# Kernel tuning notes

Measured on AMD Instinct MI355X. Metric: run time of the kernel, lower is better.

## Reference

```python
import jax, jax.numpy as jnp
import numpy as np

B, N, H = 32, 512, 128
LN_EPS = 1e-5

def _layernorm(x):
    # LayerNorm over last dim, no affine (elementwise_affine=False)
    mu = jnp.mean(x, axis=-1, keepdims=True)
    var = jnp.var(x, axis=-1, keepdims=True)
    return (x - mu) * jax.lax.rsqrt(var + LN_EPS)

def setup_inputs() -> dict:
    key = jax.random.key(0)
    k0, k1, k2, k3 = jax.random.split(key, 4)
    s = jax.random.normal(k0, (B, N, H), dtype=jnp.float32)
    ev = jax.random.normal(k1, (B, N, N, 3), dtype=jnp.float32)
    mask = (jax.random.uniform(k2, (B, N, N, 1)) > 0.5).astype(jnp.float32)
    W1 = jax.random.normal(k3, (H, H), dtype=jnp.float32) / np.sqrt(H)
    b1 = jnp.zeros((H,), dtype=jnp.float32)
    return {"s": s, "ev": ev, "mask": mask, "W1": W1, "b1": b1}

def reference(s, ev, mask, W1, b1):
    # lin1: Linear -> LayerNorm (no affine) -> SiLU
    h = jnp.einsum('bnh,kh->bnk', s, W1) + b1          # (B, N, H)
    h = jax.nn.silu(_layernorm(h))
    # Fused CFConv: v[b,i,c,d] = sum_j mask[b,i,j] * ev[b,i,j,c] * h[b,j,d]
    mev = ev * mask                                     # (B, N, N, 3)
    v = jnp.einsum('bijc,bjd->bicd', mev, h)            # (B, N, 3, H)
    return v
```

## Files before the change

kernel.cpp:

```cpp
#include <hip/hip_runtime.h>
#include <hip/hip_bf16.h>

#define B_ 32
#define N_ 512
#define H_ 128

typedef float f32x4 __attribute__((ext_vector_type(4)));
typedef short short8 __attribute__((ext_vector_type(8)));
typedef short short4v __attribute__((ext_vector_type(4)));

static __device__ __forceinline__ float bf2f(unsigned short u) {
  union { unsigned int ui; float f; } x;
  x.ui = ((unsigned int)u) << 16;
  return x.f;
}
static __device__ __forceinline__ unsigned short f2bf(float f) {
  __hip_bfloat16 h = __float2bfloat16(f);
  return *reinterpret_cast<unsigned short*>(&h);
}

__global__ __launch_bounds__(256) void lin_ln_silu_kernel(
    const float* __restrict__ s, const float* __restrict__ W1,
    const float* __restrict__ b1, unsigned short* __restrict__ h_t) {
  __shared__ float s_sh[32 * 132];
  __shared__ unsigned short w_sh[128 * 132];
  __shared__ unsigned short ht_sh[128 * 40];
  const int t = threadIdx.x;
  const int b = blockIdx.y;
  const int n0 = blockIdx.x * 32;

#pragma unroll
  for (int r = 0; r < 16; ++r) {
    int q = t + 256 * r;
    int d = q >> 5, part = q & 31;
    float4 v = *reinterpret_cast<const float4*>(W1 + d * H_ + part * 4);
    short4v w;
    w.x = (short)f2bf(v.x); w.y = (short)f2bf(v.y);
    w.z = (short)f2bf(v.z); w.w = (short)f2bf(v.w);
    *reinterpret_cast<short4v*>(&w_sh[d * 132 + part * 4]) = w;
  }
#pragma unroll
  for (int r = 0; r < 4; ++r) {
    int q = t + 256 * r;
    int n = q >> 5, part = q & 31;
    float4 v = *reinterpret_cast<const float4*>(
        s + ((size_t)b * N_ + n0 + n) * H_ + part * 4);
    *reinterpret_cast<float4*>(&s_sh[n * 132 + part * 4]) = v;
  }
  __syncthreads();

  const int a = t & 15;
  const int g = t >> 4;
  float acc[2][8];
#pragma unroll
  for (int nn = 0; nn < 2; ++nn)
#pragma unroll
    for (int dd = 0; dd < 8; ++dd) acc[nn][dd] = 0.f;

  float bias[8];
#pragma unroll
  for (int dd = 0; dd < 8; ++dd) bias[dd] = b1[dd * 16 + a];

  for (int k = 0; k < 128; k += 4) {
    float wf[8][4];
#pragma unroll
    for (int dd = 0; dd < 8; ++dd) {
      short4v wv =
          *reinterpret_cast<const short4v*>(&w_sh[(dd * 16 + a) * 132 + k]);
      wf[dd][0] = bf2f((unsigned short)wv.x);
      wf[dd][1] = bf2f((unsigned short)wv.y);
      wf[dd][2] = bf2f((unsigned short)wv.z);
      wf[dd][3] = bf2f((unsigned short)wv.w);
    }
#pragma unroll
    for (int nn = 0; nn < 2; ++nn) {
      float4 sv =
          *reinterpret_cast<const float4*>(&s_sh[(nn * 16 + g) * 132 + k]);
#pragma unroll
      for (int dd = 0; dd < 8; ++dd) {
        acc[nn][dd] += sv.x * wf[dd][0] + sv.y * wf[dd][1] +
                       sv.z * wf[dd][2] + sv.w * wf[dd][3];
      }
    }
  }

#pragma unroll
  for (int nn = 0; nn < 2; ++nn) {
    float s1 = 0.f, s2 = 0.f;
#pragma unroll
    for (int dd = 0; dd < 8; ++dd) {
      float x = acc[nn][dd] + bias[dd];
      acc[nn][dd] = x;
      s1 += x;
      s2 += x * x;
    }
#pragma unroll
    for (int off = 8; off >= 1; off >>= 1) {
      s1 += __shfl_xor(s1, off);
      s2 += __shfl_xor(s2, off);
    }
    float mean = s1 * (1.f / 128.f);
    float var = s2 * (1.f / 128.f) - mean * mean;
    float rs = rsqrtf(var + 1e-5f);
#pragma unroll
    for (int dd = 0; dd < 8; ++dd) {
      float x = (acc[nn][dd] - mean) * rs;
      float y = x / (1.f + __expf(-x));
      ht_sh[(dd * 16 + a) * 40 + nn * 16 + g] = f2bf(y);
    }
  }
  __syncthreads();

#pragma unroll
  for (int r = 0; r < 2; ++r) {
    int q = t + 256 * r;
    int d = q >> 2, part = q & 3;
    float4 v = *reinterpret_cast<const float4*>(&ht_sh[d * 40 + part * 8]);
    *reinterpret_cast<float4*>(
        h_t + ((size_t)b * 128 + d) * 512 + n0 + part * 8) = v;
  }
}

__global__ __launch_bounds__(256) void cfconv_mfma_kernel(
    const float* __restrict__ ev, const float* __restrict__ mask,
    const unsigned short* __restrict__ h_t, float* __restrict__ out) {
  __shared__ unsigned short ph[48 * 72];
  __shared__ unsigned short hh[128 * 72];
  const int t = threadIdx.x;
  const int b = blockIdx.y;
  const int i0 = blockIdx.x * 16;
  const int lane = t & 63;
  const int w = t >> 6;
  const int l15 = lane & 15;
  const int quad = lane >> 4;

  f32x4 acc[3][2];
#pragma unroll
  for (int mt = 0; mt < 3; ++mt)
#pragma unroll
    for (int nt = 0; nt < 2; ++nt)
#pragma unroll
      for (int e = 0; e < 4; ++e) acc[mt][nt][e] = 0.f;

  for (int j0 = 0; j0 < N_; j0 += 64) {
    __syncthreads();

#pragma unroll
    for (int r = 0; r < 4; ++r) {
      int q = t + 256 * r;
      int d = q >> 3, p8 = q & 7;
      float4 v = *reinterpret_cast<const float4*>(
          h_t + ((size_t)b * 128 + d) * 512 + j0 + p8 * 8);
      *reinterpret_cast<float4*>(&hh[d * 72 + p8 * 8]) = v;
    }

#pragma unroll
    for (int r = 0; r < 3; ++r) {
      int q = t + 256 * r;
      int i = q / 48, part = q % 48;
      int f0 = part * 4;
      const float* evbase =
          ev + ((size_t)((b * N_ + i0 + i)) * N_ + j0) * 3;
      float4 e4 = *reinterpret_cast<const float4*>(evbase + f0);
      const float* mrow = mask + (size_t)(b * N_ + i0 + i) * N_ + j0;
      int jlo = f0 / 3, jhi = (f0 + 3) / 3;
      float mlo = mrow[jlo], mhi = mrow[jhi];
      float evv[4] = {e4.x, e4.y, e4.z, e4.w};
#pragma unroll
      for (int e = 0; e < 4; ++e) {
        int f = f0 + e;
        int j = f / 3, c = f - 3 * j;
        float m = (j == jlo) ? mlo : mhi;
        ph[(c * 16 + i) * 72 + j] = f2bf(evv[e] * m);
      }
    }
    __syncthreads();

#pragma unroll
    for (int ks = 0; ks < 2; ++ks) {
      short8 av[3], bv[2];
#pragma unroll
      for (int mt = 0; mt < 3; ++mt)
        av[mt] = *reinterpret_cast<const short8*>(
            &ph[(mt * 16 + l15) * 72 + ks * 32 + quad * 8]);
#pragma unroll
      for (int nt = 0; nt < 2; ++nt) {
        int d = w * 32 + nt * 16 + l15;
        bv[nt] = *reinterpret_cast<const short8*>(
            &hh[d * 72 + ks * 32 + quad * 8]);
      }
#pragma unroll
      for (int mt = 0; mt < 3; ++mt)
#pragma unroll
        for (int nt = 0; nt < 2; ++nt)
          acc[mt][nt] = __builtin_amdgcn_mfma_f32_16x16x32_bf16(
              av[mt], bv[nt], acc[mt][nt], 0, 0, 0);
    }
  }

#pragma unroll
  for (int mt = 0; mt < 3; ++mt) {
#pragma unroll
    for (int nt = 0; nt < 2; ++nt) {
      int d = w * 32 + nt * 16 + l15;
#pragma unroll
      for (int r = 0; r < 4; ++r) {
        int i = i0 + quad * 4 + r;
        out[(((size_t)b * N_ + i) * 3 + mt) * H_ + d] = acc[mt][nt][r];
      }
    }
  }
}

extern "C" void kernel_launch(void* const* d_in, const int* in_sizes, int n_in,
                              void* d_out, int out_size, void* d_ws,
                              size_t ws_size, hipStream_t stream) {
  const float* s = (const float*)d_in[0];
  const float* ev = (const float*)d_in[1];
  const float* mask = (const float*)d_in[2];
  const float* W1 = (const float*)d_in[3];
  const float* b1 = (const float*)d_in[4];
  float* out = (float*)d_out;
  unsigned short* h_t = (unsigned short*)d_ws;

  lin_ln_silu_kernel<<<dim3(N_ / 32, B_), 256, 0, stream>>>(s, W1, b1, h_t);
  cfconv_mfma_kernel<<<dim3(N_ / 16, B_), 256, 0, stream>>>(ev, mask, h_t, out);
}
```

Measured before the change: 214.1 us.

## Split CFConv feature dim across blocks and vectorize ev/mask staging loads

The CFConv kernel now launches two 128-thread blocks per (batch, 16-row) tile, each covering half of the 128 feature columns, which doubles the grid and halves the shared h tile. The ev/mask staging is rewritten so each thread loads three float4 of ev and one float4 of mask for four j values, then writes packed short4 bf16 values per channel instead of scalar stores. The aim is more parallelism, wider global loads and fewer scattered LDS writes. In exchange, every ev/mask tile is now read and converted twice, once by each feature-half block, which adds HBM/L2 traffic on the dominant input.

```diff
diff --git a/kernel.cpp b/kernel.cpp
--- a/kernel.cpp
+++ b/kernel.cpp
@@ -121,14 +121,15 @@
   }
 }
 
-__global__ __launch_bounds__(256) void cfconv_mfma_kernel(
+__global__ __launch_bounds__(128) void cfconv_mfma_kernel(
     const float* __restrict__ ev, const float* __restrict__ mask,
     const unsigned short* __restrict__ h_t, float* __restrict__ out) {
   __shared__ unsigned short ph[48 * 72];
-  __shared__ unsigned short hh[128 * 72];
+  __shared__ unsigned short hh[64 * 72];
   const int t = threadIdx.x;
-  const int b = blockIdx.y;
-  const int i0 = blockIdx.x * 16;
+  const int dhalf = blockIdx.x * 64;
+  const int i0 = blockIdx.y * 16;
+  const int b = blockIdx.z;
   const int lane = t & 63;
   const int w = t >> 6;
   const int l15 = lane & 15;
@@ -147,31 +148,36 @@
 
 #pragma unroll
     for (int r = 0; r < 4; ++r) {
-      int q = t + 256 * r;
+      int q = t + 128 * r;
       int d = q >> 3, p8 = q & 7;
       float4 v = *reinterpret_cast<const float4*>(
-          h_t + ((size_t)b * 128 + d) * 512 + j0 + p8 * 8);
+          h_t + ((size_t)b * 128 + dhalf + d) * 512 + j0 + p8 * 8);
       *reinterpret_cast<float4*>(&hh[d * 72 + p8 * 8]) = v;
     }
 
 #pragma unroll
-    for (int r = 0; r < 3; ++r) {
-      int q = t + 256 * r;
-      int i = q / 48, part = q % 48;
-      int f0 = part * 4;
-      const float* evbase =
-          ev + ((size_t)((b * N_ + i0 + i)) * N_ + j0) * 3;
-      float4 e4 = *reinterpret_cast<const float4*>(evbase + f0);
-      const float* mrow = mask + (size_t)(b * N_ + i0 + i) * N_ + j0;
-      int jlo = f0 / 3, jhi = (f0 + 3) / 3;
-      float mlo = mrow[jlo], mhi = mrow[jhi];
-      float evv[4] = {e4.x, e4.y, e4.z, e4.w};
-#pragma unroll
-      for (int e = 0; e < 4; ++e) {
-        int f = f0 + e;
-        int j = f / 3, c = f - 3 * j;
-        float m = (j == jlo) ? mlo : mhi;
-        ph[(c * 16 + i) * 72 + j] = f2bf(evv[e] * m);
+    for (int r = 0; r < 2; ++r) {
+      int task = t + 128 * r;
+      int i = task >> 4, jq = task & 15;
+      int j = jq * 4;
+      const float* evb =
+          ev + ((size_t)(b * N_ + i0 + i) * N_ + j0 + j) * 3;
+      float4 e0 = *reinterpret_cast<const float4*>(evb);
+      float4 e1 = *reinterpret_cast<const float4*>(evb + 4);
+      float4 e2 = *reinterpret_cast<const float4*>(evb + 8);
+      float4 m4 = *reinterpret_cast<const float4*>(
+          mask + (size_t)(b * N_ + i0 + i) * N_ + j0 + j);
+      float f[12] = {e0.x, e0.y, e0.z, e0.w, e1.x, e1.y,
+                     e1.z, e1.w, e2.x, e2.y, e2.z, e2.w};
+      float mm[4] = {m4.x, m4.y, m4.z, m4.w};
+#pragma unroll
+      for (int c = 0; c < 3; ++c) {
+        short4v wv;
+        wv.x = (short)f2bf(f[0 * 3 + c] * mm[0]);
+        wv.y = (short)f2bf(f[1 * 3 + c] * mm[1]);
+        wv.z = (short)f2bf(f[2 * 3 + c] * mm[2]);
+        wv.w = (short)f2bf(f[3 * 3 + c] * mm[3]);
+        *reinterpret_cast<short4v*>(&ph[(c * 16 + i) * 72 + j]) = wv;
       }
     }
     __syncthreads();
@@ -202,7 +208,7 @@
   for (int mt = 0; mt < 3; ++mt) {
 #pragma unroll
     for (int nt = 0; nt < 2; ++nt) {
-      int d = w * 32 + nt * 16 + l15;
+      int d = dhalf + w * 32 + nt * 16 + l15;
 #pragma unroll
       for (int r = 0; r < 4; ++r) {
         int i = i0 + quad * 4 + r;
@@ -224,5 +230,6 @@
   unsigned short* h_t = (unsigned short*)d_ws;
 
   lin_ln_silu_kernel<<<dim3(N_ / 32, B_), 256, 0, stream>>>(s, W1, b1, h_t);
-  cfconv_mfma_kernel<<<dim3(N_ / 16, B_), 256, 0, stream>>>(ev, mask, h_t, out);
-}
+  cfconv_mfma_kernel<<<dim3(2, N_ / 16, B_), 128, 0, stream>>>(ev, mask, h_t,
+                                                               out);
+}
```

Result: no change. 214.9 us (+0.4%).

## Use MFMA for linear layer and store h in pre-swizzled MFMA fragment layout

Applied to the files above, without the earlier changes.

The first kernel now converts s and W1 to bf16 in MFMA fragment order and computes the linear layer with bf16 MFMA instead of scalar FMA. LayerNorm statistics are reduced across two waves through shared memory. h is written in a fragment-ready global layout, so the cfconv kernel loads B operands straight from global without staging them in LDS. The cfconv grid is split over d-halves with 128-thread blocks. The split means each block re-reads the ev/mask tile, doubling that traffic, and the s input is now rounded to bf16.

```diff
diff --git a/kernel.cpp b/kernel.cpp
--- a/kernel.cpp
+++ b/kernel.cpp
@@ -9,207 +9,215 @@
 typedef short short8 __attribute__((ext_vector_type(8)));
 typedef short short4v __attribute__((ext_vector_type(4)));
 
-static __device__ __forceinline__ float bf2f(unsigned short u) {
-  union { unsigned int ui; float f; } x;
-  x.ui = ((unsigned int)u) << 16;
-  return x.f;
-}
 static __device__ __forceinline__ unsigned short f2bf(float f) {
   __hip_bfloat16 h = __float2bfloat16(f);
   return *reinterpret_cast<unsigned short*>(&h);
 }
 
-__global__ __launch_bounds__(256) void lin_ln_silu_kernel(
+
+__global__ __launch_bounds__(256, 2) void lin_ln_silu_kernel(
     const float* __restrict__ s, const float* __restrict__ W1,
-    const float* __restrict__ b1, unsigned short* __restrict__ h_t) {
-  __shared__ float s_sh[32 * 132];
-  __shared__ unsigned short w_sh[128 * 132];
-  __shared__ unsigned short ht_sh[128 * 40];
+    const float* __restrict__ b1, unsigned short* __restrict__ hfrag) {
+  __shared__ unsigned short afr[2 * 4 * 512];
+  __shared__ unsigned short bfr[8 * 4 * 512];
+  __shared__ unsigned short trans[128 * 34];
+  __shared__ float lnb[2][32][2];
   const int t = threadIdx.x;
+  const int n0 = blockIdx.x * 32;
   const int b = blockIdx.y;
-  const int n0 = blockIdx.x * 32;
-
-#pragma unroll
-  for (int r = 0; r < 16; ++r) {
-    int q = t + 256 * r;
-    int d = q >> 5, part = q & 31;
-    float4 v = *reinterpret_cast<const float4*>(W1 + d * H_ + part * 4);
-    short4v w;
-    w.x = (short)f2bf(v.x); w.y = (short)f2bf(v.y);
-    w.z = (short)f2bf(v.z); w.w = (short)f2bf(v.w);
-    *reinterpret_cast<short4v*>(&w_sh[d * 132 + part * 4]) = w;
-  }
-#pragma unroll
-  for (int r = 0; r < 4; ++r) {
-    int q = t + 256 * r;
-    int n = q >> 5, part = q & 31;
-    float4 v = *reinterpret_cast<const float4*>(
-        s + ((size_t)b * N_ + n0 + n) * H_ + part * 4);
-    *reinterpret_cast<float4*>(&s_sh[n * 132 + part * 4]) = v;
-  }
-  __syncthreads();
-
-  const int a = t & 15;
-  const int g = t >> 4;
-  float acc[2][8];
-#pragma unroll
-  for (int nn = 0; nn < 2; ++nn)
-#pragma unroll
-    for (int dd = 0; dd < 8; ++dd) acc[nn][dd] = 0.f;
-
-  float bias[8];
-#pragma unroll
-  for (int dd = 0; dd < 8; ++dd) bias[dd] = b1[dd * 16 + a];
-
-  for (int k = 0; k < 128; k += 4) {
-    float wf[8][4];
-#pragma unroll
-    for (int dd = 0; dd < 8; ++dd) {
-      short4v wv =
-          *reinterpret_cast<const short4v*>(&w_sh[(dd * 16 + a) * 132 + k]);
-      wf[dd][0] = bf2f((unsigned short)wv.x);
-      wf[dd][1] = bf2f((unsigned short)wv.y);
-      wf[dd][2] = bf2f((unsigned short)wv.z);
-      wf[dd][3] = bf2f((unsigned short)wv.w);
-    }
-#pragma unroll
-    for (int nn = 0; nn < 2; ++nn) {
-      float4 sv =
-          *reinterpret_cast<const float4*>(&s_sh[(nn * 16 + g) * 132 + k]);
-#pragma unroll
-      for (int dd = 0; dd < 8; ++dd) {
-        acc[nn][dd] += sv.x * wf[dd][0] + sv.y * wf[dd][1] +
-                       sv.z * wf[dd][2] + sv.w * wf[dd][3];
-      }
-    }
-  }
-
-#pragma unroll
-  for (int nn = 0; nn < 2; ++nn) {
-    float s1 = 0.f, s2 = 0.f;
-#pragma unroll
-    for (int dd = 0; dd < 8; ++dd) {
-      float x = acc[nn][dd] + bias[dd];
-      acc[nn][dd] = x;
-      s1 += x;
-      s2 += x * x;
-    }
-#pragma unroll
-    for (int off = 8; off >= 1; off >>= 1) {
-      s1 += __shfl_xor(s1, off);
-      s2 += __shfl_xor(s2, off);
-    }
-    float mean = s1 * (1.f / 128.f);
-    float var = s2 * (1.f / 128.f) - mean * mean;
-    float rs = rsqrtf(var + 1e-5f);
-#pragma unroll
-    for (int dd = 0; dd < 8; ++dd) {
-      float x = (acc[nn][dd] - mean) * rs;
-      float y = x / (1.f + __expf(-x));
-      ht_sh[(dd * 16 + a) * 40 + nn * 16 + g] = f2bf(y);
-    }
-  }
-  __syncthreads();
-
-#pragma unroll
-  for (int r = 0; r < 2; ++r) {
-    int q = t + 256 * r;
-    int d = q >> 2, part = q & 3;
-    float4 v = *reinterpret_cast<const float4*>(&ht_sh[d * 40 + part * 8]);
-    *reinterpret_cast<float4*>(
-        h_t + ((size_t)b * 128 + d) * 512 + n0 + part * 8) = v;
-  }
-}
-
-__global__ __launch_bounds__(256) void cfconv_mfma_kernel(
-    const float* __restrict__ ev, const float* __restrict__ mask,
-    const unsigned short* __restrict__ h_t, float* __restrict__ out) {
-  __shared__ unsigned short ph[48 * 72];
-  __shared__ unsigned short hh[128 * 72];
-  const int t = threadIdx.x;
-  const int b = blockIdx.y;
-  const int i0 = blockIdx.x * 16;
   const int lane = t & 63;
   const int w = t >> 6;
   const int l15 = lane & 15;
   const int quad = lane >> 4;
 
+#pragma unroll
+  for (int rep = 0; rep < 4; ++rep) {
+    int q = t + 256 * rep;
+    int n = q >> 5, k = (q & 31) * 4;
+    float4 v = *reinterpret_cast<const float4*>(
+        s + ((size_t)(b * N_ + n0 + n)) * H_ + k);
+    short4v sv;
+    sv.x = (short)f2bf(v.x); sv.y = (short)f2bf(v.y);
+    sv.z = (short)f2bf(v.z); sv.w = (short)f2bf(v.w);
+    int mt = n >> 4, ks = k >> 5, qd = (k >> 3) & 3, e0 = k & 7;
+    *reinterpret_cast<short4v*>(
+        &afr[((mt * 4 + ks) * 64 + qd * 16 + (n & 15)) * 8 + e0]) = sv;
+  }
+#pragma unroll
+  for (int rep = 0; rep < 16; ++rep) {
+    int q = t + 256 * rep;
+    int d = q >> 5, k = (q & 31) * 4;
+    float4 v = *reinterpret_cast<const float4*>(W1 + (size_t)d * H_ + k);
+    short4v sv;
+    sv.x = (short)f2bf(v.x); sv.y = (short)f2bf(v.y);
+    sv.z = (short)f2bf(v.z); sv.w = (short)f2bf(v.w);
+    int nt = d >> 4, ks = k >> 5, qd = (k >> 3) & 3, e0 = k & 7;
+    *reinterpret_cast<short4v*>(
+        &bfr[((nt * 4 + ks) * 64 + qd * 16 + (d & 15)) * 8 + e0]) = sv;
+  }
+  __syncthreads();
+
+  const int mt = w >> 1, dhalf = w & 1;
+  f32x4 acc[4];
+#pragma unroll
+  for (int nt2 = 0; nt2 < 4; ++nt2)
+#pragma unroll
+    for (int e = 0; e < 4; ++e) acc[nt2][e] = 0.f;
+
+#pragma unroll
+  for (int ks = 0; ks < 4; ++ks) {
+    short8 av =
+        *reinterpret_cast<const short8*>(&afr[((mt * 4 + ks) * 64 + lane) * 8]);
+#pragma unroll
+    for (int nt2 = 0; nt2 < 4; ++nt2) {
+      short8 bv = *reinterpret_cast<const short8*>(
+          &bfr[(((dhalf * 4 + nt2) * 4 + ks) * 64 + lane) * 8]);
+      acc[nt2] =
+          __builtin_amdgcn_mfma_f32_16x16x32_bf16(av, bv, acc[nt2], 0, 0, 0);
+    }
+  }
+
+  float bb[4];
+#pragma unroll
+  for (int nt2 = 0; nt2 < 4; ++nt2)
+    bb[nt2] = b1[dhalf * 64 + nt2 * 16 + l15];
+
+#pragma unroll
+  for (int rr = 0; rr < 4; ++rr) {
+    float s1 = 0.f, s2 = 0.f;
+#pragma unroll
+    for (int nt2 = 0; nt2 < 4; ++nt2) {
+      float x = acc[nt2][rr] + bb[nt2];
+      acc[nt2][rr] = x;
+      s1 += x;
+      s2 += x * x;
+    }
+#pragma unroll
+    for (int off = 8; off >= 1; off >>= 1) {
+      s1 += __shfl_xor(s1, off);
+      s2 += __shfl_xor(s2, off);
+    }
+    int row = mt * 16 + quad * 4 + rr;
+    if (l15 == 0) {
+      lnb[dhalf][row][0] = s1;
+      lnb[dhalf][row][1] = s2;
+    }
+  }
+  __syncthreads();
+
+#pragma unroll
+  for (int rr = 0; rr < 4; ++rr) {
+    int row = mt * 16 + quad * 4 + rr;
+    float s1 = lnb[0][row][0] + lnb[1][row][0];
+    float s2 = lnb[0][row][1] + lnb[1][row][1];
+    float mean = s1 * (1.f / 128.f);
+    float var = s2 * (1.f / 128.f) - mean * mean;
+    float rs = rsqrtf(var + 1e-5f);
+#pragma unroll
+    for (int nt2 = 0; nt2 < 4; ++nt2) {
+      float x = (acc[nt2][rr] - mean) * rs;
+      float y = x / (1.f + __expf(-x));
+      trans[(dhalf * 64 + nt2 * 16 + l15) * 34 + row] = f2bf(y);
+    }
+  }
+  __syncthreads();
+
+#pragma unroll
+  for (int rep = 0; rep < 2; ++rep) {
+    int q = t + 256 * rep;
+    int d = q >> 2, k2 = q & 3;
+    short8 v = *reinterpret_cast<const short8*>(&trans[d * 34 + k2 * 8]);
+    int n = n0 + k2 * 8;
+    int KS = n >> 5, q16 = (n >> 3) & 3;
+    *reinterpret_cast<short8*>(
+        hfrag + (size_t)b * 65536 +
+        (size_t)(((d >> 4) * 16 + KS) * 64 + q16 * 16 + (d & 15)) * 8) = v;
+  }
+}
+
+__global__ __launch_bounds__(128, 5) void cfconv_mfma_kernel(
+    const float* __restrict__ ev, const float* __restrict__ mask,
+    const unsigned short* __restrict__ hfrag, float* __restrict__ out) {
+  __shared__ unsigned short ph[3 * 2 * 512];
+  const int t = threadIdx.x;
+  const int i0 = blockIdx.x * 16;
+  const int dh4 = blockIdx.y * 4;
+  const int b = blockIdx.z;
+  const int lane = t & 63;
+  const int w = t >> 6;
+  const int l15 = lane & 15;
+  const int quad = lane >> 4;
+
+  const float* evb = ev + (size_t)(b * N_ + i0) * N_ * 3;
+  const float* mb = mask + (size_t)(b * N_ + i0) * N_;
+  const unsigned short* hfb = hfrag + (size_t)b * 65536;
+
   f32x4 acc[3][2];
 #pragma unroll
-  for (int mt = 0; mt < 3; ++mt)
-#pragma unroll
-    for (int nt = 0; nt < 2; ++nt)
-#pragma unroll
-      for (int e = 0; e < 4; ++e) acc[mt][nt][e] = 0.f;
-
-  for (int j0 = 0; j0 < N_; j0 += 64) {
-    __syncthreads();
-
-#pragma unroll
-    for (int r = 0; r < 4; ++r) {
-      int q = t + 256 * r;
-      int d = q >> 3, p8 = q & 7;
-      float4 v = *reinterpret_cast<const float4*>(
-          h_t + ((size_t)b * 128 + d) * 512 + j0 + p8 * 8);
-      *reinterpret_cast<float4*>(&hh[d * 72 + p8 * 8]) = v;
-    }
-
-#pragma unroll
-    for (int r = 0; r < 3; ++r) {
-      int q = t + 256 * r;
-      int i = q / 48, part = q % 48;
-      int f0 = part * 4;
-      const float* evbase =
-          ev + ((size_t)((b * N_ + i0 + i)) * N_ + j0) * 3;
-      float4 e4 = *reinterpret_cast<const float4*>(evbase + f0);
-      const float* mrow = mask + (size_t)(b * N_ + i0 + i) * N_ + j0;
-      int jlo = f0 / 3, jhi = (f0 + 3) / 3;
-      float mlo = mrow[jlo], mhi = mrow[jhi];
-      float evv[4] = {e4.x, e4.y, e4.z, e4.w};
+  for (int c = 0; c < 3; ++c)
+#pragma unroll
+    for (int p = 0; p < 2; ++p)
+#pragma unroll
+      for (int e = 0; e < 4; ++e) acc[c][p][e] = 0.f;
+
+  for (int r = 0; r < 8; ++r) {
+    const int j0 = r * 64;
+    if (r) __syncthreads();
+
+#pragma unroll
+    for (int rep = 0; rep < 6; ++rep) {
+      int ch = t + 128 * rep;
+      int i = ch / 48;
+      int f0 = (ch % 48) * 4;
+      float4 e4 = *reinterpret_cast<const float4*>(
+          evb + ((size_t)i * N_ + j0) * 3 + f0);
+      int jl0 = f0 / 3;
+      float mlo = mb[(size_t)i * N_ + j0 + jl0];
+      float mhi = mb[(size_t)i * N_ + j0 + jl0 + 1];
+      float fe[4] = {e4.x, e4.y, e4.z, e4.w};
 #pragma unroll
       for (int e = 0; e < 4; ++e) {
         int f = f0 + e;
-        int j = f / 3, c = f - 3 * j;
-        float m = (j == jlo) ? mlo : mhi;
-        ph[(c * 16 + i) * 72 + j] = f2bf(evv[e] * m);
+        int j = f / 3;
+        int c = f - j * 3;
+        float m = (j == jl0) ? mlo : mhi;
+        ph[c * 1024 + (j >> 5) * 512 + ((j >> 3) & 3) * 128 + i * 8 +
+           (j & 7)] = f2bf(fe[e] * m);
       }
     }
     __syncthreads();
 
 #pragma unroll
     for (int ks = 0; ks < 2; ++ks) {
-      short8 av[3], bv[2];
-#pragma unroll
-      for (int mt = 0; mt < 3; ++mt)
-        av[mt] = *reinterpret_cast<const short8*>(
-            &ph[(mt * 16 + l15) * 72 + ks * 32 + quad * 8]);
-#pragma unroll
-      for (int nt = 0; nt < 2; ++nt) {
-        int d = w * 32 + nt * 16 + l15;
-        bv[nt] = *reinterpret_cast<const short8*>(
-            &hh[d * 72 + ks * 32 + quad * 8]);
+      short8 av[3];
+#pragma unroll
+      for (int c = 0; c < 3; ++c)
+        av[c] = *reinterpret_cast<const short8*>(
+            &ph[(c * 2 + ks) * 512 + lane * 8]);
+#pragma unroll
+      for (int p = 0; p < 2; ++p) {
+        const int NT = dh4 + w * 2 + p;
+        short8 bv = *reinterpret_cast<const short8*>(
+            hfb + (size_t)((NT * 16 + r * 2 + ks) * 64 + lane) * 8);
+#pragma unroll
+        for (int c = 0; c < 3; ++c)
+          acc[c][p] = __builtin_amdgcn_mfma_f32_16x16x32_bf16(av[c], bv,
+                                                              acc[c][p], 0, 0, 0);
       }
-#pragma unroll
-      for (int mt = 0; mt < 3; ++mt)
-#pragma unroll
-        for (int nt = 0; nt < 2; ++nt)
-          acc[mt][nt] = __builtin_amdgcn_mfma_f32_16x16x32_bf16(
-              av[mt], bv[nt], acc[mt][nt], 0, 0, 0);
-    }
-  }
-
-#pragma unroll
-  for (int mt = 0; mt < 3; ++mt) {
-#pragma unroll
-    for (int nt = 0; nt < 2; ++nt) {
-      int d = w * 32 + nt * 16 + l15;
-#pragma unroll
-      for (int r = 0; r < 4; ++r) {
-        int i = i0 + quad * 4 + r;
-        out[(((size_t)b * N_ + i) * 3 + mt) * H_ + d] = acc[mt][nt][r];
+    }
+  }
+
+#pragma unroll
+  for (int c = 0; c < 3; ++c)
+#pragma unroll
+    for (int p = 0; p < 2; ++p) {
+      const int d = (dh4 + w * 2 + p) * 16 + l15;
+#pragma unroll
+      for (int rr = 0; rr < 4; ++rr) {
+        const int i = i0 + quad * 4 + rr;
+        out[(((size_t)b * N_ + i) * 3 + c) * H_ + d] = acc[c][p][rr];
       }
     }
-  }
 }
 
 extern "C" void kernel_launch(void* const* d_in, const int* in_sizes, int n_in,
@@ -221,8 +229,9 @@
   const float* W1 = (const float*)d_in[3];
   const float* b1 = (const float*)d_in[4];
   float* out = (float*)d_out;
-  unsigned short* h_t = (unsigned short*)d_ws;
-
-  lin_ln_silu_kernel<<<dim3(N_ / 32, B_), 256, 0, stream>>>(s, W1, b1, h_t);
-  cfconv_mfma_kernel<<<dim3(N_ / 16, B_), 256, 0, stream>>>(ev, mask, h_t, out);
-}
+  unsigned short* hfrag = (unsigned short*)d_ws;
+
+  lin_ln_silu_kernel<<<dim3(N_ / 32, B_), 256, 0, stream>>>(s, W1, b1, hfrag);
+  cfconv_mfma_kernel<<<dim3(N_ / 16, 2, B_), 128, 0, stream>>>(ev, mask, hfrag,
+                                                               out);
+}
```

New measurement: 219.5 us. +2.5%, slower.
